# Optimization experiments

Measured on AMD Instinct MI355X. Metric: run time of the kernel, lower is better.

The kernel has to match this reference:

```python
import jax, jax.numpy as jnp
import numpy as np

B, S, WP = 64, 128, 18          # batch, words/sentence, padded chars/word
K = 3                            # char window size (module constant)
E = 128                          # embedding_dim
H = 256                          # hidden_dim
L = 4                            # cnn out channels (l=4 in module)
V = 50000                        # vocab size
A = 100                          # alphabet size
T = 50                           # tagset size


def setup_inputs() -> dict:
    key = jax.random.key(0)
    ks = jax.random.split(key, 14)
    n = lambda k, *sh: jax.random.normal(k, sh, dtype=jnp.float32) * 0.1
    return {
        "char_ids": jax.random.randint(ks[0], (B, S, WP), 0, A),
        "word_ids": jax.random.randint(ks[1], (B, S), 0, V),
        "char_emb": n(ks[2], A, E),
        "word_emb": n(ks[3], V + 1, E),
        "cnn_w": n(ks[4], L, K * E),
        "cnn_b": n(ks[5], L),
        "wih_f": n(ks[6], 4 * H, E),
        "whh_f": n(ks[7], 4 * H, H),
        "b_f": n(ks[8], 4 * H),
        "wih_b": n(ks[9], 4 * H, E),
        "whh_b": n(ks[10], 4 * H, H),
        "b_b": n(ks[11], 4 * H),
        "out_w": n(ks[12], T, 2 * H),
        "out_b": n(ks[13], T),
    }


def _lstm(x, Wih, Whh, b, reverse):
    # x: [S, B, E] -> hs: [S, B, H]; PyTorch gate order i, f, g, o
    hdim = Whh.shape[1]

    def step(carry, xt):
        h, c = carry
        z = xt @ Wih.T + h @ Whh.T + b
        i, f, g, o = jnp.split(z, 4, axis=-1)
        c = jax.nn.sigmoid(f) * c + jax.nn.sigmoid(i) * jnp.tanh(g)
        h = jax.nn.sigmoid(o) * jnp.tanh(c)
        return (h, c), h

    h0 = jnp.zeros((x.shape[1], hdim), x.dtype)
    _, hs = jax.lax.scan(step, (h0, h0), x, reverse=reverse)
    return hs


def reference(char_ids, word_ids, char_emb, word_emb, cnn_w, cnn_b,
              wih_f, whh_f, b_f, wih_b, whh_b, b_b, out_w, out_b):
    # --- per-word char CNN + max-pool (fully batched over B, S, positions) ---
    ce = char_emb[char_ids]                        # [B, S, WP, E]
    W = WP - (K - 1)                               # window positions per word
    windows = jnp.concatenate([ce[:, :, i:i + W] for i in range(K)], axis=-1)  # [B,S,W,K*E]
    phi = jnp.einsum('bswd,cd->bswc', windows, cnn_w) + cnn_b                  # [B,S,W,L]
    char_reprs = phi.max(axis=2)                   # [B, S, L] (unused by tag path, as in original)

    # --- word embeddings -> BiLSTM -> linear -> log_softmax over seq dim ---
    we = word_emb[word_ids]                        # [B, S, E]
    x = we.transpose(1, 0, 2)                      # [S, B, E]
    hf = _lstm(x, wih_f, whh_f, b_f, reverse=False)
    hb = _lstm(x, wih_b, whh_b, b_b, reverse=True)
    lstm_out = jnp.concatenate([hf, hb], axis=-1).transpose(1, 0, 2)  # [B, S, 2H]
    tag_space = lstm_out @ out_w.T + out_b         # [B, S, T]
    tag_scores = jax.nn.log_softmax(tag_space, axis=1)  # dim=1 as in original
    return tag_scores, char_reprs
```

## Files before the change

### kernel.cpp

```cpp
#include <hip/hip_runtime.h>
#include <hip/hip_bf16.h>

#define B_  64
#define S_  128
#define WP_ 18
#define K_  3
#define E_  128
#define H_  256
#define L_  4
#define T_  50

typedef __hip_bfloat16 bf16;

__device__ __forceinline__ float b2f(bf16 x) { return __bfloat162float(x); }
__device__ __forceinline__ bf16  f2b(float x) { return __float2bfloat16(x); }

__device__ __forceinline__ float fast_sigmoid(float x) {
    return 1.f / (1.f + __expf(-x));
}
__device__ __forceinline__ float fast_tanh(float x) {
    float a = fminf(fmaxf(2.f * x, -30.f), 30.f);
    float e = __expf(a);
    return (e - 1.f) / (e + 1.f);
}
__device__ __forceinline__ unsigned int pack2(float lo, float hi) {
    bf16 l = f2b(lo), h = f2b(hi);
    unsigned short ls = *(unsigned short*)&l, hs = *(unsigned short*)&h;
    return ((unsigned int)hs << 16) | ls;
}

#define DOT2(z, w, h) asm("v_dot2_f32_bf16 %0, %1, %2, %0" : "+v"(z) : "v"(w), "v"(h))
#define PIN4(V_) asm volatile("" : "+v"((V_).x), "+v"((V_).y), "+v"((V_).z), "+v"((V_).w))

__global__ void k_prep(const float* __restrict__ whh_f, const float* __restrict__ whh_b,
                       const float* __restrict__ wih_f, const float* __restrict__ wih_b,
                       unsigned int* __restrict__ wp_f, unsigned int* __restrict__ wp_b,
                       unsigned int* __restrict__ wihT2_f, unsigned int* __restrict__ wihT2_b) {
    int blk = blockIdx.x, t = threadIdx.x;
    if (blk < 1024) {
        const float* src   = (blk < 512) ? whh_f : whh_b;
        unsigned int* dst  = (blk < 512) ? wp_f  : wp_b;
        int d = ((blk & 511) << 8) + t;
        int m2 = d >> 11, rem = d & 2047;
        int u = rem >> 2, e2 = rem & 3;
        int i = u >> 1, p2 = u & 1;
        int g = m2 >> 4, kk2 = m2 & 15;
        int col = (g << 8) + i;
        int k = (p2 << 7) + (kk2 << 3) + (e2 << 1);
        float2 sv = *(const float2*)(src + col * 256 + k);
        dst[d] = pack2(sv.x, sv.y);
    } else {
        int id = blk - 1024;
        const float* src  = (id < 256) ? wih_f   : wih_b;
        unsigned int* dst = (id < 256) ? wihT2_f : wihT2_b;
        int d = ((id & 255) << 8) + t;
        int kp = d >> 10, j = d & 1023;
        float2 sv = *(const float2*)(src + j * 128 + 2 * kp);
        dst[d] = pack2(sv.x, sv.y);
    }
}

__global__ void k_input_proj(const int* __restrict__ word_ids,
                             const float* __restrict__ word_emb,
                             const unsigned int* __restrict__ wihT2_f, const float* __restrict__ b_f,
                             const unsigned int* __restrict__ wihT2_b, const float* __restrict__ b_b,
                             bf16* __restrict__ igq_f, bf16* __restrict__ igq_b) {
    int dir = blockIdx.y;
    const unsigned int* wihT2 = dir ? wihT2_b : wihT2_f;
    const float* bb  = dir ? b_b   : b_f;
    bf16* igq        = dir ? igq_b : igq_f;
    __shared__ unsigned int x2[32][64];
    int t  = threadIdx.x;
    int r0 = blockIdx.x * 32;
    for (int u = t; u < 32 * 64; u += 512) {
        int rr = u >> 6, ep = u & 63;
        int r = r0 + rr;
        int s = r >> 6, b = r & 63;
        int wid = word_ids[b * S_ + s];
        float2 ev = *(const float2*)(word_emb + (size_t)wid * E_ + 2 * ep);
        x2[rr][ep] = pack2(ev.x, ev.y);
    }
    __syncthreads();
    int j = t & 255, jh = t >> 8;
    float acc[2][32];
    #pragma unroll
    for (int c2 = 0; c2 < 2; ++c2) {
        float bv = bb[j + (2 * jh + c2) * 256];
        #pragma unroll
        for (int rr = 0; rr < 32; ++rr) acc[c2][rr] = bv;
    }
    for (int kp = 0; kp < 64; ++kp) {
        unsigned int wv0 = wihT2[kp * 1024 + j + (2 * jh) * 256];
        unsigned int wv1 = wihT2[kp * 1024 + j + (2 * jh + 1) * 256];
        #pragma unroll
        for (int rr = 0; rr < 32; ++rr) {
            unsigned int xp = x2[rr][kp];
            DOT2(acc[0][rr], wv0, xp);
            DOT2(acc[1][rr], wv1, xp);
        }
    }
    #pragma unroll
    for (int rr = 0; rr < 32; ++rr)
        *(unsigned int*)(igq + (size_t)(r0 + rr) * 1024 + j * 4 + 2 * jh) =
            pack2(acc[0][rr], acc[1][rr]);
}

__global__ __launch_bounds__(512, 2) void k_lstm_cnn(
        const bf16* __restrict__ igq_f, const bf16* __restrict__ igq_b,
        const uint4* __restrict__ wp_f, const uint4* __restrict__ wp_b,
        unsigned int* __restrict__ hfp, unsigned int* __restrict__ hbp,
        const int* __restrict__ char_ids, const float* __restrict__ char_emb,
        const float* __restrict__ cnn_w, const float* __restrict__ cnn_b,
        float* __restrict__ out_char) {
    __shared__ uint4 wlds[9216];
    __shared__ __align__(16) unsigned int hpbuf[2][160];

    int t = threadIdx.x;

    if (blockIdx.x < 128) {
        int b   = blockIdx.x & 63;
        int dir = blockIdx.x >> 6;
        const bf16* igq  = dir ? igq_b : igq_f;
        const uint4* wp  = dir ? wp_b  : wp_f;
        unsigned int* hs = dir ? hbp   : hfp;

        int i = t >> 1, p2 = t & 1;

        for (int v = t; v < 4096; v += 512) wlds[v] = wp[56 * 512 + v];
        if (t < 320) ((unsigned int*)hpbuf)[t] = 0;
        float c_reg = 0.f;

        uint4 wreg[56];
        #pragma unroll
        for (int m = 0; m < 56; ++m) {
            wreg[m] = wp[m * 512 + t];
            PIN4(wreg[m]);
        }
        __syncthreads();

        int cur = 0;
        int s0 = dir ? (S_ - 1) : 0;
        uint2 igu = *(const uint2*)&igq[((size_t)s0 * B_ + b) * 1024 + i * 4];

        for (int step = 0; step < S_; ++step) {
            int s = dir ? (S_ - 1 - step) : step;

            float z0 = 0.f, z1 = 0.f, z2 = 0.f, z3 = 0.f;
            if (p2 == 0) {
                z0 = __uint_as_float(igu.x << 16);
                z1 = __uint_as_float(igu.x & 0xffff0000u);
                z2 = __uint_as_float(igu.y << 16);
                z3 = __uint_as_float(igu.y & 0xffff0000u);
            }
            const char* hpc = (const char*)hpbuf[cur];
            #pragma unroll
            for (int kk = 0; kk < 16; ++kk) {
                uint4 hv = *(const uint4*)(hpc + (p2 * 2 + (kk >> 3)) * 144 + (kk & 7) * 16);
                {   uint4 wv = wreg[kk];
                    DOT2(z0, wv.x, hv.x); DOT2(z0, wv.y, hv.y);
                    DOT2(z0, wv.z, hv.z); DOT2(z0, wv.w, hv.w); }
                {   uint4 wv = wreg[16 + kk];
                    DOT2(z1, wv.x, hv.x); DOT2(z1, wv.y, hv.y);
                    DOT2(z1, wv.z, hv.z); DOT2(z1, wv.w, hv.w); }
                {   uint4 wv = wreg[32 + kk];
                    DOT2(z2, wv.x, hv.x); DOT2(z2, wv.y, hv.y);
                    DOT2(z2, wv.z, hv.z); DOT2(z2, wv.w, hv.w); }
                {   uint4 wv = (kk < 8) ? wreg[48 + kk] : wlds[(kk - 8) * 512 + t];
                    DOT2(z3, wv.x, hv.x); DOT2(z3, wv.y, hv.y);
                    DOT2(z3, wv.z, hv.z); DOT2(z3, wv.w, hv.w); }
            }
            if (step + 1 < S_) {
                int sn = dir ? (S_ - 2 - step) : (step + 1);
                igu = *(const uint2*)&igq[((size_t)sn * B_ + b) * 1024 + i * 4];
            }
            z0 += __shfl_xor(z0, 1);
            z1 += __shfl_xor(z1, 1);
            z2 += __shfl_xor(z2, 1);
            z3 += __shfl_xor(z3, 1);
            if (p2 == 0) {
                float si = fast_sigmoid(z0);
                float sf = fast_sigmoid(z1);
                float tg = fast_tanh(z2);
                float so = fast_sigmoid(z3);
                c_reg = sf * c_reg + si * tg;
                float hn = so * fast_tanh(c_reg);
                char* dstb = (char*)hpbuf[cur ^ 1] + (i >> 6) * 144 + ((i >> 1) & 31) * 4 + (i & 1) * 2;
                *(bf16*)dstb = f2b(hn);
            }
            __syncthreads();
            if (t < 128) {
                hs[((size_t)s * B_ + b) * 128 + t] =
                    hpbuf[cur ^ 1][(t >> 5) * 36 + (t & 31)];
            }
            cur ^= 1;
        }
    } else {
        unsigned int* pool_u = (unsigned int*)wlds;
        float*        pool_f = (float*)wlds;
        int blkc = blockIdx.x - 128;

        for (int u = t; u < 4 * 192; u += 512) {
            int c = u / 192, pe = u % 192;
            pool_u[c * 196 + pe] = pack2(cnn_w[c * 384 + 2 * pe], cnn_w[c * 384 + 2 * pe + 1]);
        }
        if (t < 4) pool_f[784 + t] = cnn_b[t];
        __syncthreads();

        int wv = t >> 6, lane = t & 63;
        unsigned int* cew = pool_u + 800 + wv * 1224;
        int pos = lane >> 2, c = lane & 3;

        #pragma unroll 1
        for (int j = 0; j < 8; ++j) {
            int word = (blkc * 8 + wv) * 8 + j;
            const int* ids = char_ids + word * WP_;
            for (int row = 0; row < WP_; ++row) {
                float2 ev = *(const float2*)(char_emb + (size_t)ids[row] * 128 + 2 * lane);
                cew[row * 68 + lane] = pack2(ev.x, ev.y);
            }
            float acc = 0.f;
            #pragma unroll
            for (int i = 0; i < K_; ++i) {
                const uint4* cr = (const uint4*)(cew + (pos + i) * 68);
                const uint4* wr = (const uint4*)(pool_u + c * 196 + i * 64);
                #pragma unroll
                for (int q = 0; q < 16; ++q) {
                    uint4 cv = cr[q], wq = wr[q];
                    DOT2(acc, wq.x, cv.x); DOT2(acc, wq.y, cv.y);
                    DOT2(acc, wq.z, cv.z); DOT2(acc, wq.w, cv.w);
                }
            }
            acc += pool_f[784 + c];
            #pragma unroll
            for (int off = 4; off < 64; off <<= 1) acc = fmaxf(acc, __shfl_xor(acc, off));
            if (lane < L_) out_char[(size_t)word * L_ + lane] = acc;
        }
    }
}

__global__ __launch_bounds__(1024) void k_tag_linear(
        const unsigned int* __restrict__ hfp, const unsigned int* __restrict__ hbp,
        const float* __restrict__ out_w, const float* __restrict__ out_b,
        float* __restrict__ tag) {
    __shared__ unsigned int ow[50 * 257];
    __shared__ unsigned int hv[16][256];
    int bs0 = blockIdx.x * 16;
    int t = threadIdx.x;
    for (int u = t; u < 12800; u += 1024) {
        int tt = u >> 8, kp = u & 255;
        float2 wv = *(const float2*)(out_w + tt * 512 + 2 * kp);
        ow[tt * 257 + kp] = pack2(wv.x, wv.y);
    }
    for (int u = t; u < 16 * 256; u += 1024) {
        int w = u >> 8, q = u & 255;
        int bs = bs0 + w;
        int b = bs >> 7, s = bs & 127;
        const unsigned int* src = (q < 128) ? hfp : hbp;
        hv[w][q] = src[((size_t)s * B_ + b) * 128 + (q & 127)];
    }
    __syncthreads();
    int w = t >> 6, tt = t & 63;
    if (tt < T_) {
        int bs = bs0 + w;
        int b = bs >> 7, s = bs & 127;
        float acc = out_b[tt];
        const unsigned int* owr = &ow[tt * 257];
        const unsigned int* hvr = hv[w];
        #pragma unroll 8
        for (int kp = 0; kp < 256; ++kp) DOT2(acc, owr[kp], hvr[kp]);
        tag[((size_t)b * T_ + tt) * S_ + s] = acc;
    }
}

__global__ void k_log_softmax(const float* __restrict__ tag, float* __restrict__ out) {
    int wid  = (blockIdx.x * 256 + threadIdx.x) >> 6;
    int lane = threadIdx.x & 63;
    if (wid >= B_ * T_) return;
    int b = wid / T_, t = wid % T_;
    const float* row = tag + (size_t)wid * S_;
    float v0 = row[lane], v1 = row[lane + 64];
    float m = fmaxf(v0, v1);
    #pragma unroll
    for (int off = 32; off; off >>= 1) m = fmaxf(m, __shfl_xor(m, off));
    float e = expf(v0 - m) + expf(v1 - m);
    #pragma unroll
    for (int off = 32; off; off >>= 1) e += __shfl_xor(e, off);
    float lse = m + logf(e);
    out[((size_t)b * S_ + lane)      * T_ + t] = v0 - lse;
    out[((size_t)b * S_ + lane + 64) * T_ + t] = v1 - lse;
}

extern "C" void kernel_launch(void* const* d_in, const int* in_sizes, int n_in,
                              void* d_out, int out_size, void* d_ws, size_t ws_size,
                              hipStream_t stream) {
    const int*   char_ids = (const int*)d_in[0];
    const int*   word_ids = (const int*)d_in[1];
    const float* char_emb = (const float*)d_in[2];
    const float* word_emb = (const float*)d_in[3];
    const float* cnn_w    = (const float*)d_in[4];
    const float* cnn_b    = (const float*)d_in[5];
    const float* wih_f    = (const float*)d_in[6];
    const float* whh_f    = (const float*)d_in[7];
    const float* b_f      = (const float*)d_in[8];
    const float* wih_b    = (const float*)d_in[9];
    const float* whh_b    = (const float*)d_in[10];
    const float* b_b      = (const float*)d_in[11];
    const float* out_w    = (const float*)d_in[12];
    const float* out_b    = (const float*)d_in[13];
    float* out = (float*)d_out;
    char* ws   = (char*)d_ws;

    size_t o = 0;
    unsigned int* wihT2_f = (unsigned int*)(ws + o); o += (size_t)64 * 1024 * 4;
    unsigned int* wihT2_b = (unsigned int*)(ws + o); o += (size_t)64 * 1024 * 4;
    unsigned int* wp_f    = (unsigned int*)(ws + o); o += (size_t)1024 * 128 * 4;
    unsigned int* wp_b    = (unsigned int*)(ws + o); o += (size_t)1024 * 128 * 4;
    bf16* igq_f  = (bf16*)(ws + o); o += (size_t)S_ * B_ * 1024 * 2;
    bf16* igq_b  = (bf16*)(ws + o); o += (size_t)S_ * B_ * 1024 * 2;
    unsigned int* hfp = (unsigned int*)(ws + o); o += (size_t)S_ * B_ * 128 * 4;
    unsigned int* hbp = (unsigned int*)(ws + o); o += (size_t)S_ * B_ * 128 * 4;
    float* tag   = (float*)(ws + o); o += (size_t)B_ * T_ * S_ * 4;

    k_prep<<<1536, 256, 0, stream>>>(whh_f, whh_b, wih_f, wih_b,
                                     wp_f, wp_b, wihT2_f, wihT2_b);
    k_input_proj<<<dim3(256, 2), 512, 0, stream>>>(word_ids, word_emb,
                                                   wihT2_f, b_f, wihT2_b, b_b, igq_f, igq_b);
    k_lstm_cnn<<<256, 512, 0, stream>>>(igq_f, igq_b,
                                        (const uint4*)wp_f, (const uint4*)wp_b, hfp, hbp,
                                        char_ids, char_emb, cnn_w, cnn_b,
                                        out + (size_t)B_ * S_ * T_);
    k_tag_linear<<<B_ * S_ / 16, 1024, 0, stream>>>(hfp, hbp, out_w, out_b, tag);
    k_log_softmax<<<(B_ * T_ + 3) / 4, 256, 0, stream>>>(tag, out);
}
```

Measured before the change: 333.8 us.

## Fuse tag linear and log-softmax into one per-batch kernel

Merges the output projection and the sequence-dim log-softmax into a single kernel with one block per batch row, so the tag scores stay in LDS instead of round-tripping through a global buffer. This removes one launch and the intermediate write and read. In exchange only 64 blocks run (down from 512), which cuts parallelism, and each block still reloads the full output weight. LDS use rises to roughly 141 KB per block.

```diff
diff --git a/kernel.cpp b/kernel.cpp
--- a/kernel.cpp
+++ b/kernel.cpp
@@ -238,56 +238,57 @@
     }
 }
 
-__global__ __launch_bounds__(1024) void k_tag_linear(
+__global__ __launch_bounds__(1024) void k_tag_sm(
         const unsigned int* __restrict__ hfp, const unsigned int* __restrict__ hbp,
         const float* __restrict__ out_w, const float* __restrict__ out_b,
-        float* __restrict__ tag) {
+        float* __restrict__ out) {
     __shared__ unsigned int ow[50 * 257];
-    __shared__ unsigned int hv[16][256];
-    int bs0 = blockIdx.x * 16;
+    __shared__ unsigned int hv[64][256];
+    __shared__ float tb[50][128];
+    int b = blockIdx.x;
     int t = threadIdx.x;
+
     for (int u = t; u < 12800; u += 1024) {
         int tt = u >> 8, kp = u & 255;
         float2 wv = *(const float2*)(out_w + tt * 512 + 2 * kp);
         ow[tt * 257 + kp] = pack2(wv.x, wv.y);
     }
-    for (int u = t; u < 16 * 256; u += 1024) {
-        int w = u >> 8, q = u & 255;
-        int bs = bs0 + w;
-        int b = bs >> 7, s = bs & 127;
-        const unsigned int* src = (q < 128) ? hfp : hbp;
-        hv[w][q] = src[((size_t)s * B_ + b) * 128 + (q & 127)];
+
+    for (int chunk = 0; chunk < 2; ++chunk) {
+        int sbase = chunk * 64;
+        __syncthreads();
+        for (int u = t; u < 64 * 256; u += 1024) {
+            int sl = u >> 8, q = u & 255;
+            int s = sbase + sl;
+            const unsigned int* src = (q < 128) ? hfp : hbp;
+            hv[sl][q] = src[((size_t)s * B_ + b) * 128 + (q & 127)];
+        }
+        __syncthreads();
+        for (int u = t; u < 50 * 64; u += 1024) {
+            int tt = u >> 6, sl = u & 63;
+            float acc = out_b[tt];
+            const unsigned int* owr = &ow[tt * 257];
+            const unsigned int* hvr = hv[sl];
+            #pragma unroll 8
+            for (int kp = 0; kp < 256; ++kp) DOT2(acc, owr[kp], hvr[kp]);
+            tb[tt][sbase + sl] = acc;
+        }
     }
     __syncthreads();
-    int w = t >> 6, tt = t & 63;
-    if (tt < T_) {
-        int bs = bs0 + w;
-        int b = bs >> 7, s = bs & 127;
-        float acc = out_b[tt];
-        const unsigned int* owr = &ow[tt * 257];
-        const unsigned int* hvr = hv[w];
-        #pragma unroll 8
-        for (int kp = 0; kp < 256; ++kp) DOT2(acc, owr[kp], hvr[kp]);
-        tag[((size_t)b * T_ + tt) * S_ + s] = acc;
-    }
-}
-
-__global__ void k_log_softmax(const float* __restrict__ tag, float* __restrict__ out) {
-    int wid  = (blockIdx.x * 256 + threadIdx.x) >> 6;
-    int lane = threadIdx.x & 63;
-    if (wid >= B_ * T_) return;
-    int b = wid / T_, t = wid % T_;
-    const float* row = tag + (size_t)wid * S_;
-    float v0 = row[lane], v1 = row[lane + 64];
-    float m = fmaxf(v0, v1);
-    #pragma unroll
-    for (int off = 32; off; off >>= 1) m = fmaxf(m, __shfl_xor(m, off));
-    float e = expf(v0 - m) + expf(v1 - m);
-    #pragma unroll
-    for (int off = 32; off; off >>= 1) e += __shfl_xor(e, off);
-    float lse = m + logf(e);
-    out[((size_t)b * S_ + lane)      * T_ + t] = v0 - lse;
-    out[((size_t)b * S_ + lane + 64) * T_ + t] = v1 - lse;
+
+    int wv = t >> 6, lane = t & 63;
+    for (int row = wv; row < T_; row += 16) {
+        float v0 = tb[row][lane], v1 = tb[row][lane + 64];
+        float m = fmaxf(v0, v1);
+        #pragma unroll
+        for (int off = 32; off; off >>= 1) m = fmaxf(m, __shfl_xor(m, off));
+        float e = expf(v0 - m) + expf(v1 - m);
+        #pragma unroll
+        for (int off = 32; off; off >>= 1) e += __shfl_xor(e, off);
+        float lse = m + logf(e);
+        out[((size_t)b * S_ + lane)      * T_ + row] = v0 - lse;
+        out[((size_t)b * S_ + lane + 64) * T_ + row] = v1 - lse;
+    }
 }
 
 extern "C" void kernel_launch(void* const* d_in, const int* in_sizes, int n_in,
@@ -319,7 +320,6 @@
     bf16* igq_b  = (bf16*)(ws + o); o += (size_t)S_ * B_ * 1024 * 2;
     unsigned int* hfp = (unsigned int*)(ws + o); o += (size_t)S_ * B_ * 128 * 4;
     unsigned int* hbp = (unsigned int*)(ws + o); o += (size_t)S_ * B_ * 128 * 4;
-    float* tag   = (float*)(ws + o); o += (size_t)B_ * T_ * S_ * 4;
 
     k_prep<<<1536, 256, 0, stream>>>(whh_f, whh_b, wih_f, wih_b,
                                      wp_f, wp_b, wihT2_f, wihT2_b);
@@ -329,6 +329,5 @@
                                         (const uint4*)wp_f, (const uint4*)wp_b, hfp, hbp,
                                         char_ids, char_emb, cnn_w, cnn_b,
                                         out + (size_t)B_ * S_ * T_);
-    k_tag_linear<<<B_ * S_ / 16, 1024, 0, stream>>>(hfp, hbp, out_w, out_b, tag);
-    k_log_softmax<<<(B_ * T_ + 3) / 4, 256, 0, stream>>>(tag, out);
-}
+    k_tag_sm<<<B_, 1024, 0, stream>>>(hfp, hbp, out_w, out_b, out);
+}
```

Result: slower. 1.032 ms (+209.2%).
